# Optimization experiments

Hardware: AMD Instinct MI355X
Metric: run time of the kernel (lower is better)

## Reference

```python
import jax, jax.numpy as jnp
import numpy as np

NUM_HEADS = 8
ATTENTION_SPAN = 128
LOOKAHEAD = True
NEG_INF = -1e9  # tf.keras Softmax mask adder


def setup_inputs() -> dict:
    key = jax.random.key(0)
    k1, k2, k3 = jax.random.split(key, 3)
    B, S, D = 4, 2048, 512
    x = jax.random.normal(k1, (B, S, D), dtype=jnp.float32)
    w_qkv = jax.random.normal(k2, (D, 3 * D), dtype=jnp.float32) * (D ** -0.5)
    w_proj = jax.random.normal(k3, (D, D), dtype=jnp.float32) * (D ** -0.5)
    return {"x": x, "w_qkv": w_qkv, "w_proj": w_proj}


def _band_mask(S: int) -> jnp.ndarray:
    idx = jnp.arange(S)
    m = jnp.abs(idx[None, :] - idx[:, None]) <= ATTENTION_SPAN
    if not LOOKAHEAD:
        m = m & (idx[None, :] <= idx[:, None])
    return m  # [S, S] bool


def reference(x, w_qkv, w_proj):
    B, S, D = x.shape
    H = NUM_HEADS
    hd = D // H
    scale = D ** -0.5  # NOTE: source scales by full dim, not head_dim

    qkv = x @ w_qkv                                   # [B,S,3D]
    qkv = qkv.reshape(B, S, H, 3 * hd).transpose(0, 2, 1, 3)  # [B,H,S,3hd]
    q, k, v = jnp.split(qkv, 3, axis=-1)              # each [B,H,S,hd]

    scores = jnp.einsum('bhqd,bhkd->bhqk', q, k) * scale  # [B,H,S,S]
    mask = _band_mask(S)[None, None, :, :]
    scores = scores + (1.0 - mask.astype(scores.dtype)) * NEG_INF
    attn = jax.nn.softmax(scores, axis=-1)

    out = jnp.einsum('bhqk,bhkd->bhqd', attn, v)      # [B,H,S,hd]
    out = out.transpose(0, 2, 1, 3).reshape(B, S, D)
    return out @ w_proj
```

## Files before the change

### kernel.cpp

```cpp
#include <hip/hip_runtime.h>

typedef unsigned short u16;
typedef __attribute__((ext_vector_type(8))) short s16x8;
typedef __attribute__((ext_vector_type(4))) float f32x4;

#define MFMA16(a, b, c) __builtin_amdgcn_mfma_f32_16x16x32_bf16((a), (b), (c), 0, 0, 0)

__device__ __forceinline__ u16 f2bf(float f) {
  unsigned u = __float_as_uint(f);
  u += 0x7fffu + ((u >> 16) & 1u);
  return (u16)(u >> 16);
}

__device__ __forceinline__ void gld_lds16(const void* g, void* l) {
  __builtin_amdgcn_global_load_lds(
      (const __attribute__((address_space(1))) void*)g,
      (__attribute__((address_space(3))) void*)l, 16, 0, 0);
}

__global__ __launch_bounds__(256) void prep(const float* __restrict__ X,
                                            const float* __restrict__ Wqkv,
                                            const float* __restrict__ Wproj,
                                            u16* __restrict__ Xb,
                                            u16* __restrict__ wqT,
                                            u16* __restrict__ wpT) {
  const int bid = blockIdx.x;
  if (bid < 2048) {
    size_t idx = (size_t)bid * 256 + threadIdx.x;
    const float4 f0 = *(const float4*)(X + idx * 8);
    const float4 f1 = *(const float4*)(X + idx * 8 + 4);
    float fs[8] = {f0.x, f0.y, f0.z, f0.w, f1.x, f1.y, f1.z, f1.w};
    s16x8 hv;
#pragma unroll
    for (int j = 0; j < 8; ++j) hv[j] = (short)f2bf(fs[j]);
    *(s16x8*)(Xb + idx * 8) = hv;
  } else if (bid < 2432) {
    int idx = (bid - 2048) * 256 + threadIdx.x;
    int n = idx % 1536;
    int kc = idx / 1536;
    int t = n >> 9, ct = n & 511, h = ct >> 6, d = ct & 63;
    int src_c = h * 192 + t * 64 + d;
    s16x8 hv;
#pragma unroll
    for (int i = 0; i < 8; ++i) hv[i] = (short)f2bf(Wqkv[(size_t)(kc * 8 + i) * 1536 + src_c]);
    *(s16x8*)(wqT + (size_t)n * 512 + (size_t)kc * 8) = hv;
  } else {
    int idx = (bid - 2432) * 256 + threadIdx.x;
    int n = idx % 512;
    int kc = idx / 512;
    s16x8 hv;
#pragma unroll
    for (int i = 0; i < 8; ++i) hv[i] = (short)f2bf(Wproj[(size_t)(kc * 8 + i) * 512 + n]);
    *(s16x8*)(wpT + (size_t)n * 512 + (size_t)kc * 8) = hv;
  }
}

template <int EPI, int NCOL>
__global__ __launch_bounds__(256) void gemm_bf16(
    const u16* __restrict__ A, const u16* __restrict__ B,
    float* __restrict__ OUT,
    u16* __restrict__ qo, u16* __restrict__ ko, u16* __restrict__ vto) {
  __shared__ u16 LDS[EPI ? 16640 : 16384];
  u16* SA = LDS;
  u16* SB = LDS + 8192;
  const int tid = threadIdx.x;
  const int w = tid >> 6, lane = tid & 63;
  const int l15 = lane & 15, l4 = lane >> 4;
  const int bid0 = blockIdx.x;
  const int work = (bid0 & 7) * (8 * NCOL) + (bid0 >> 3);
  const int bx = work / NCOL;
  const int by = work % NCOL;
  const int row0 = bx * 128;
  const int col0 = by * 128;
  const int wr = w >> 1, wc = w & 1;

  const int lrow = lane >> 2, lslot = lane & 3;
  const int srcoff = lrow * 1024 + ((lslot ^ (lrow & 3)) << 4);
  const char* pA = (const char*)A + (size_t)(row0 + w * 32) * 1024 + srcoff;
  const char* pB = (const char*)B + (size_t)(col0 + w * 32) * 1024 + srcoff;
  u16* sAw = SA + (w * 32) * 32;
  u16* sBw = SB + (w * 32) * 32;

#define STAGE(t_, b_)                                             \
  do {                                                            \
    const int kbb = (t_)*64;                                      \
    gld_lds16(pA + kbb,         sAw + (b_)*4096);                 \
    gld_lds16(pA + 16384 + kbb, sAw + (b_)*4096 + 512);           \
    gld_lds16(pB + kbb,         sBw + (b_)*4096);                 \
    gld_lds16(pB + 16384 + kbb, sBw + (b_)*4096 + 512);           \
  } while (0)

  const f32x4 fz = {0.f, 0.f, 0.f, 0.f};
  f32x4 acc[4][4];
  for (int a = 0; a < 4; ++a)
    for (int b = 0; b < 4; ++b) acc[a][b] = fz;

  STAGE(0, 0);
  __syncthreads();

  for (int t = 0; t < 16; ++t) {
    const int cur = t & 1;
    if (t + 1 < 16) STAGE(t + 1, cur ^ 1);
    s16x8 af[4], bf[4];
#pragma unroll
    for (int mi = 0; mi < 4; ++mi) {
      const int r = wr * 64 + mi * 16 + l15;
      const int sl = l4 ^ (r & 3);
      af[mi] = *(const s16x8*)&SA[cur * 4096 + r * 32 + sl * 8];
    }
#pragma unroll
    for (int nj = 0; nj < 4; ++nj) {
      const int r = wc * 64 + nj * 16 + l15;
      const int sl = l4 ^ (r & 3);
      bf[nj] = *(const s16x8*)&SB[cur * 4096 + r * 32 + sl * 8];
    }
#pragma unroll
    for (int nj = 0; nj < 4; ++nj)
#pragma unroll
      for (int mi = 0; mi < 4; ++mi) acc[mi][nj] = MFMA16(af[mi], bf[nj], acc[mi][nj]);
    __syncthreads();
  }
#undef STAGE

  if (EPI == 0) {
#pragma unroll
    for (int mi = 0; mi < 4; ++mi)
#pragma unroll
      for (int nj = 0; nj < 4; ++nj)
#pragma unroll
        for (int rg = 0; rg < 4; ++rg) {
          int r_g = row0 + wr * 64 + mi * 16 + l4 * 4 + rg;
          int c_g = col0 + wc * 64 + nj * 16 + l15;
          OUT[(size_t)r_g * 512 + c_g] = acc[mi][nj][rg];
        }
    return;
  }

  const int b = row0 >> 11, srow = row0 & 2047;
  if (by < 8) {
    const int isq = (by < 4);
    const float QS = 0.06375874f;
    u16* dst = isq ? qo : ko;
#pragma unroll
    for (int mi = 0; mi < 4; ++mi)
#pragma unroll
      for (int nj = 0; nj < 4; ++nj)
#pragma unroll
        for (int rg = 0; rg < 4; ++rg) {
          float v = acc[mi][nj][rg];
          if (isq) v *= QS;
          int s = srow + wr * 64 + mi * 16 + l4 * 4 + rg;
          int ct = ((by & 3) * 128 + wc * 64 + nj * 16 + l15);
          int h = ct >> 6, d = ct & 63;
          dst[(((size_t)b * 8 + h) * 2048 + s) * 64 + d] = f2bf(v);
        }
  } else {
#pragma unroll
    for (int mi = 0; mi < 4; ++mi)
#pragma unroll
      for (int nj = 0; nj < 4; ++nj)
#pragma unroll
        for (int rg = 0; rg < 4; ++rg) {
          int c = wc * 64 + nj * 16 + l15;
          int s = wr * 64 + mi * 16 + l4 * 4 + rg;
          LDS[c * 130 + s] = f2bf(acc[mi][nj][rg]);
        }
    __syncthreads();
    const unsigned* LDSw = (const unsigned*)LDS;
    int c = tid >> 1, sh = tid & 1;
    int ct = (by - 8) * 128 + c;
    int h = ct >> 6, d = ct & 63;
    size_t o = (((size_t)b * 8 + h) * 64 + d) * 2048 + srow + sh * 64;
    unsigned wbuf[32];
#pragma unroll
    for (int p = 0; p < 32; ++p) wbuf[p] = LDSw[c * 65 + sh * 32 + p];
#pragma unroll
    for (int j = 0; j < 8; ++j) {
      uint4 u = {wbuf[j * 4], wbuf[j * 4 + 1], wbuf[j * 4 + 2], wbuf[j * 4 + 3]};
      *(uint4*)(vto + o + j * 8) = u;
    }
  }
}

__global__ __launch_bounds__(512, 6) void attn_kernel(
    const u16* __restrict__ q, const u16* __restrict__ k,
    const u16* __restrict__ vt, u16* __restrict__ ao) {
  __shared__ u16 KT[2][64 * 64];
  __shared__ u16 VT[2][64 * 64];
  __shared__ u16 Ph[8][16 * 64];
  const int tid = threadIdx.x;
  const int w = tid >> 6, lane = tid & 63;
  const int l15 = lane & 15, l4 = lane >> 4;
  const int bid0 = blockIdx.x;
  const int bid = (bid0 & 7) * 64 + (bid0 >> 3);
  const int qt = bid & 15, hh = (bid >> 4) & 7, b = bid >> 7;
  const size_t base = (size_t)(b * 8 + hh) * 2048 * 64;
  const int q0 = qt * 128 + w * 16;

  s16x8 qf[2];
#pragma unroll
  for (int ks = 0; ks < 2; ++ks)
    qf[ks] = *(const s16x8*)(q + base + (size_t)(q0 + l15) * 64 + ks * 32 + l4 * 8);

  const f32x4 fz = {0.f, 0.f, 0.f, 0.f};
  f32x4 O[4];
  for (int nd = 0; nd < 4; ++nd) O[nd] = fz;
  float l_acc[4] = {0.f, 0.f, 0.f, 0.f};

  const int lrow = lane >> 3, lslot = lane & 7;
  const int swzb = (lslot ^ lrow) << 4;
  const char* pK = (const char*)(k + base) + (w * 8 + lrow) * 128 + swzb;
  const char* pV = (const char*)(vt + base) + (size_t)(w * 8 + lrow) * 4096 + swzb;
  u16* dK = &KT[0][0] + w * 512;
  u16* dV = &VT[0][0] + w * 512;

#define STAGE(c_, b_)                                    \
  do {                                                   \
    gld_lds16(pK + (c_) * 8192, dK + (b_) * 4096);       \
    gld_lds16(pV + (c_) * 128,  dV + (b_) * 4096);       \
  } while (0)

  const int c0 = (2 * qt - 2) < 0 ? 0 : (2 * qt - 2);
  const int c1 = (2 * qt + 3) > 31 ? 31 : (2 * qt + 3);

  STAGE(c0, 0);
  __syncthreads();

  for (int c = c0; c <= c1; ++c) {
    const int buf = (c - c0) & 1;
    if (c < c1) STAGE(c + 1, buf ^ 1);
    const int kb = c * 64;
    const bool skip = (kb - (q0 + 15) > 128) || (q0 - (kb + 63) > 128);
    if (!skip) {
      f32x4 S[4];
      for (int nj = 0; nj < 4; ++nj) S[nj] = fz;
#pragma unroll
      for (int nj = 0; nj < 4; ++nj) {
        const int r = nj * 16 + l15;
#pragma unroll
        for (int ks = 0; ks < 2; ++ks) {
          const int sl = (ks * 4 + l4) ^ (r & 7);
          s16x8 kf = *(const s16x8*)&KT[buf][r * 64 + sl * 8];
          S[nj] = MFMA16(qf[ks], kf, S[nj]);
        }
      }
      const bool needmask = (kb + 63 - q0 > 128) || (q0 + 15 - kb > 128);
#pragma unroll
      for (int nj = 0; nj < 4; ++nj)
#pragma unroll
        for (int rg = 0; rg < 4; ++rg) {
          const int row = l4 * 4 + rg;
          const int col = nj * 16 + l15;
          float p = exp2f(S[nj][rg]);
          if (needmask) {
            int dd = (kb + col) - (q0 + row);
            if (dd > 128 || dd < -128) p = 0.f;
          }
          l_acc[rg] += p;
          const int e = (((col >> 3) ^ (row & 7)) << 3) + (col & 7);
          Ph[w][row * 64 + e] = f2bf(p);
        }
#pragma unroll
      for (int ksp = 0; ksp < 2; ++ksp) {
        const int sl0 = (ksp * 4 + l4) ^ (l15 & 7);
        s16x8 pa = *(const s16x8*)&Ph[w][l15 * 64 + sl0 * 8];
#pragma unroll
        for (int nd = 0; nd < 4; ++nd) {
          const int r = nd * 16 + l15;
          const int sl = (ksp * 4 + l4) ^ (r & 7);
          s16x8 vf = *(const s16x8*)&VT[buf][r * 64 + sl * 8];
          O[nd] = MFMA16(pa, vf, O[nd]);
        }
      }
    }
    __syncthreads();
  }
#undef STAGE

#pragma unroll
  for (int rg = 0; rg < 4; ++rg) {
    float s = l_acc[rg];
    s += __shfl_xor(s, 1);
    s += __shfl_xor(s, 2);
    s += __shfl_xor(s, 4);
    s += __shfl_xor(s, 8);
    l_acc[rg] = 1.0f / s;
  }
#pragma unroll
  for (int rg = 0; rg < 4; ++rg) {
    const int s_g = q0 + l4 * 4 + rg;
#pragma unroll
    for (int nd = 0; nd < 4; ++nd) {
      float v = O[nd][rg] * l_acc[rg];
      const int c_g = hh * 64 + nd * 16 + l15;
      ao[((size_t)b * 2048 + s_g) * 512 + c_g] = f2bf(v);
    }
  }
}

extern "C" void kernel_launch(void* const* d_in, const int* in_sizes, int n_in,
                              void* d_out, int out_size, void* d_ws, size_t ws_size,
                              hipStream_t stream) {
  const float* x = (const float*)d_in[0];
  const float* wqkv = (const float*)d_in[1];
  const float* wproj = (const float*)d_in[2];
  float* out = (float*)d_out;

  char* ws = (char*)d_ws;
  size_t off = 0;
  auto alloc = [&](size_t bytes) {
    void* p = ws + off;
    off += (bytes + 255) & ~(size_t)255;
    return p;
  };
  const size_t E = (size_t)4 * 8 * 2048 * 64;
  u16* Xb  = (u16*)alloc(E * 2);
  u16* qb  = (u16*)alloc(E * 2);
  u16* kb  = (u16*)alloc(E * 2);
  u16* vtb = (u16*)alloc(E * 2);
  u16* aob = (u16*)alloc(E * 2);
  u16* wqT = (u16*)alloc((size_t)1536 * 512 * 2);
  u16* wpT = (u16*)alloc((size_t)512 * 512 * 2);

  prep<<<dim3(2560), dim3(256), 0, stream>>>(x, wqkv, wproj, Xb, wqT, wpT);
  gemm_bf16<1, 12><<<dim3(768), dim3(256), 0, stream>>>(Xb, wqT, nullptr, qb, kb, vtb);
  attn_kernel<<<dim3(512), dim3(512), 0, stream>>>(qb, kb, vtb, aob);
  gemm_bf16<0, 4><<<dim3(256), dim3(256), 0, stream>>>(aob, wpT, out, nullptr, nullptr, nullptr);
}
```

Baseline: 64.93 us.

## Single-buffer attention K/V tiles and halve GEMM V-epilogue LDS footprint for occupancy

The attention kernel drops K/V double buffering, loading each 64-key chunk into a single LDS buffer followed by a barrier, and raises its launch bound from 6 to 8 blocks per CU. The GEMM's V-transpose epilogue now stages one 64-column half at a time, so LDS stays at the mainloop size, and the GEMM gets a 4-blocks-per-CU launch hint. The aim is to cut LDS and register use to fit more resident blocks. The cost is that the attention kernel loses its prefetch overlap and so exposes load latency on every chunk, and the epilogue adds extra barriers.

```diff
diff --git a/kernel.cpp b/kernel.cpp
--- a/kernel.cpp
+++ b/kernel.cpp
@@ -56,11 +56,11 @@
 }
 
 template <int EPI, int NCOL>
-__global__ __launch_bounds__(256) void gemm_bf16(
+__global__ __launch_bounds__(256, 4) void gemm_bf16(
     const u16* __restrict__ A, const u16* __restrict__ B,
     float* __restrict__ OUT,
     u16* __restrict__ qo, u16* __restrict__ ko, u16* __restrict__ vto) {
-  __shared__ u16 LDS[EPI ? 16640 : 16384];
+  __shared__ u16 LDS[16384];
   u16* SA = LDS;
   u16* SB = LDS + 8192;
   const int tid = threadIdx.x;
@@ -155,38 +155,45 @@
           dst[(((size_t)b * 8 + h) * 2048 + s) * 64 + d] = f2bf(v);
         }
   } else {
-#pragma unroll
-    for (int mi = 0; mi < 4; ++mi)
-#pragma unroll
-      for (int nj = 0; nj < 4; ++nj)
-#pragma unroll
-        for (int rg = 0; rg < 4; ++rg) {
-          int c = wc * 64 + nj * 16 + l15;
-          int s = wr * 64 + mi * 16 + l4 * 4 + rg;
-          LDS[c * 130 + s] = f2bf(acc[mi][nj][rg]);
-        }
-    __syncthreads();
-    const unsigned* LDSw = (const unsigned*)LDS;
-    int c = tid >> 1, sh = tid & 1;
-    int ct = (by - 8) * 128 + c;
-    int h = ct >> 6, d = ct & 63;
-    size_t o = (((size_t)b * 8 + h) * 64 + d) * 2048 + srow + sh * 64;
-    unsigned wbuf[32];
-#pragma unroll
-    for (int p = 0; p < 32; ++p) wbuf[p] = LDSw[c * 65 + sh * 32 + p];
-#pragma unroll
-    for (int j = 0; j < 8; ++j) {
-      uint4 u = {wbuf[j * 4], wbuf[j * 4 + 1], wbuf[j * 4 + 2], wbuf[j * 4 + 3]};
-      *(uint4*)(vto + o + j * 8) = u;
-    }
-  }
-}
-
-__global__ __launch_bounds__(512, 6) void attn_kernel(
+    const int vb = by - 8;
+#pragma unroll
+    for (int h = 0; h < 2; ++h) {
+      __syncthreads();
+      if (wc == h) {
+#pragma unroll
+        for (int mi = 0; mi < 4; ++mi)
+#pragma unroll
+          for (int nj = 0; nj < 4; ++nj)
+#pragma unroll
+            for (int rg = 0; rg < 4; ++rg) {
+              int cl = nj * 16 + l15;
+              int s = wr * 64 + mi * 16 + l4 * 4 + rg;
+              LDS[cl * 130 + s] = f2bf(acc[mi][nj][rg]);
+            }
+      }
+      __syncthreads();
+      const unsigned* LDSw = (const unsigned*)LDS;
+      int cl = tid >> 2, sh = tid & 3;
+      int ct = vb * 128 + h * 64 + cl;
+      int hd = ct >> 6, d = ct & 63;
+      size_t o = (((size_t)b * 8 + hd) * 64 + d) * 2048 + srow + sh * 32;
+      unsigned wbuf[16];
+#pragma unroll
+      for (int p = 0; p < 16; ++p) wbuf[p] = LDSw[cl * 65 + sh * 16 + p];
+#pragma unroll
+      for (int j = 0; j < 4; ++j) {
+        uint4 u = {wbuf[j * 4], wbuf[j * 4 + 1], wbuf[j * 4 + 2], wbuf[j * 4 + 3]};
+        *(uint4*)(vto + o + j * 8) = u;
+      }
+    }
+  }
+}
+
+__global__ __launch_bounds__(512, 8) void attn_kernel(
     const u16* __restrict__ q, const u16* __restrict__ k,
     const u16* __restrict__ vt, u16* __restrict__ ao) {
-  __shared__ u16 KT[2][64 * 64];
-  __shared__ u16 VT[2][64 * 64];
+  __shared__ u16 KT[64 * 64];
+  __shared__ u16 VT[64 * 64];
   __shared__ u16 Ph[8][16 * 64];
   const int tid = threadIdx.x;
   const int w = tid >> 6, lane = tid & 63;
@@ -211,24 +218,16 @@
   const int swzb = (lslot ^ lrow) << 4;
   const char* pK = (const char*)(k + base) + (w * 8 + lrow) * 128 + swzb;
   const char* pV = (const char*)(vt + base) + (size_t)(w * 8 + lrow) * 4096 + swzb;
-  u16* dK = &KT[0][0] + w * 512;
-  u16* dV = &VT[0][0] + w * 512;
-
-#define STAGE(c_, b_)                                    \
-  do {                                                   \
-    gld_lds16(pK + (c_) * 8192, dK + (b_) * 4096);       \
-    gld_lds16(pV + (c_) * 128,  dV + (b_) * 4096);       \
-  } while (0)
+  u16* dK = &KT[0] + w * 512;
+  u16* dV = &VT[0] + w * 512;
 
   const int c0 = (2 * qt - 2) < 0 ? 0 : (2 * qt - 2);
   const int c1 = (2 * qt + 3) > 31 ? 31 : (2 * qt + 3);
 
-  STAGE(c0, 0);
-  __syncthreads();
-
   for (int c = c0; c <= c1; ++c) {
-    const int buf = (c - c0) & 1;
-    if (c < c1) STAGE(c + 1, buf ^ 1);
+    gld_lds16(pK + c * 8192, dK);
+    gld_lds16(pV + c * 128, dV);
+    __syncthreads();
     const int kb = c * 64;
     const bool skip = (kb - (q0 + 15) > 128) || (q0 - (kb + 63) > 128);
     if (!skip) {
@@ -240,7 +239,7 @@
 #pragma unroll
         for (int ks = 0; ks < 2; ++ks) {
           const int sl = (ks * 4 + l4) ^ (r & 7);
-          s16x8 kf = *(const s16x8*)&KT[buf][r * 64 + sl * 8];
+          s16x8 kf = *(const s16x8*)&KT[r * 64 + sl * 8];
           S[nj] = MFMA16(qf[ks], kf, S[nj]);
         }
       }
@@ -268,14 +267,13 @@
         for (int nd = 0; nd < 4; ++nd) {
           const int r = nd * 16 + l15;
           const int sl = (ksp * 4 + l4) ^ (r & 7);
-          s16x8 vf = *(const s16x8*)&VT[buf][r * 64 + sl * 8];
+          s16x8 vf = *(const s16x8*)&VT[r * 64 + sl * 8];
           O[nd] = MFMA16(pa, vf, O[nd]);
         }
       }
     }
     __syncthreads();
   }
-#undef STAGE
 
 #pragma unroll
   for (int rg = 0; rg < 4; ++rg) {
```

Result: slower. 86.12 us (+32.6%).
